# Optimization experiments

Measured on AMD Instinct MI355X. Metric: run time of the kernel, lower is better.

## Reference

```python
import jax, jax.numpy as jnp
import numpy as np

N = 20000      # n_nodes
L = 4          # lamb_len (number of decay rates)
M = 64         # memory_dimension (= message_dimension)
F = 128        # node feature dim
E = 128        # embedding_dimension
B = 100000     # number of interaction events in the batch
RAW = 2 * M * L + F + 1  # 641, raw message dim
H = RAW // 2   # MLP hidden dim


def setup_inputs() -> dict:
    key = jax.random.key(0)
    ks = jax.random.split(key, 18)
    s = lambda d: 1.0 / np.sqrt(d)
    inp = {
        "node_features": jax.random.normal(ks[0], (N, F), jnp.float32),
        "memory": jax.random.normal(ks[1], (N, L, M), jnp.float32) * 0.1,
        "last_update": jnp.zeros((N,), jnp.float32),
        "lambs": jnp.array([1.0, 0.1, 0.01, 0.001], jnp.float32),
        "theta": jnp.array([0.5], jnp.float32),
        "static_emb": jax.random.normal(ks[2], (N, E), jnp.float32),
        "W1": jax.random.normal(ks[3], (H, RAW), jnp.float32) * s(RAW),
        "b1": jnp.zeros((H,), jnp.float32),
        "W2": jax.random.normal(ks[4], (M, H), jnp.float32) * s(H),
        "b2": jnp.zeros((M,), jnp.float32),
        "We": jax.random.normal(ks[5], (M, L * M), jnp.float32) * s(L * M),
        "be": jnp.zeros((M,), jnp.float32),
        "Ws": jax.random.normal(ks[6], (E, M), jnp.float32) * s(M),
        "bs": jnp.zeros((E,), jnp.float32),
        "timestamps": jax.random.uniform(ks[7], (B,), jnp.float32) * 1000.0,
        "source_nodes": jax.random.randint(ks[8], (B,), 0, N),
        "target_nodes": jax.random.randint(ks[9], (B,), 0, N),
    }
    return inp


def reference(node_features, memory, last_update, lambs, theta, static_emb,
              W1, b1, W2, b2, We, be, Ws, bs,
              timestamps, source_nodes, target_nodes):
    n, l, m = memory.shape
    b = source_nodes.shape[0]
    mem_flat = memory.reshape(n, l * m)

    # ---- temporal memory gather + raw message build: [B, RAW] ----
    src_emb = mem_flat[source_nodes]
    tgt_emb = mem_flat[target_nodes]
    raw = jnp.concatenate(
        [src_emb, tgt_emb, node_features[target_nodes],
         jnp.ones((b, 1), memory.dtype)], axis=1)

    # ---- exp_lambs aggregation per source node ----
    t_node = jax.ops.segment_max(timestamps, source_nodes, num_segments=n)
    counts = jax.ops.segment_sum(jnp.ones_like(timestamps), source_nodes,
                                 num_segments=n)
    has = counts > 0
    t_node_safe = jnp.where(has, t_node, last_update)  # latest event time per node
    dt = t_node_safe[source_nodes] - timestamps        # [B], >= 0
    w = jnp.exp(-dt[:, None] * lambs[None, :])         # [B, L] decay weights
    # decayed sum of raw messages per node, per lambda: [N, L, RAW]
    agg = jnp.stack(
        [jax.ops.segment_sum(w[:, li:li + 1] * raw, source_nodes,
                             num_segments=n) for li in range(l)], axis=1)

    # ---- MLP message function: [N, L, M] ----
    h = jax.nn.relu(jnp.einsum('nlr,hr->nlh', agg, W1) + b1)
    msg = jnp.einsum('nlh,mh->nlm', h, W2) + b2

    # ---- exp memory update ----
    decay = jnp.exp(-(t_node_safe - last_update)[:, None] * lambs[None, :])  # [N, L]
    updated = memory * decay[..., None] + jnp.where(has[:, None, None], msg, 0.0)

    # ---- embedding fusion ----
    dyn = updated.reshape(n, l * m)
    e = jax.nn.leaky_relu(dyn @ We.T + be, negative_slope=0.01)
    s = jax.nn.leaky_relu(e @ Ws.T + bs, negative_slope=0.01)
    embeddings = theta * static_emb + (1.0 - theta) * s
    return embeddings
```

## Files before the change

### kernel.cpp

```cpp
#include <hip/hip_runtime.h>

constexpr int LDIM = 4;
constexpr int MDIM = 64;
constexpr int FDIM = 128;
constexpr int EDIM = 128;
constexpr int RAWD = 641;
constexpr int HDIM = 320;
constexpr int LM   = LDIM * MDIM;
constexpr int KXY  = LM + FDIM;
constexpr int NXY  = 2 * HDIM;

typedef _Float16 f16x8 __attribute__((ext_vector_type(8)));
typedef _Float16 f16x4 __attribute__((ext_vector_type(4)));
typedef float    f32x4 __attribute__((ext_vector_type(4)));

constexpr float WSCALE  = 256.f;
constexpr float WSINV   = 1.f / 256.f;

__global__ void k_init(int* t_node_bits, int* counts, int* cursor2, int* cursor, int Nn)
{
    int n = blockIdx.x * blockDim.x + threadIdx.x;
    if (n < Nn) {
        t_node_bits[n] = 0xBF800000;
        counts[n]  = 0;
        cursor2[n] = 0;
    }
    if (n == 0) cursor[0] = 0;
}

__global__ void k_ev1(const int* __restrict__ src, const float* __restrict__ ts,
                      int* t_node_bits, int* counts, int Bev)
{
    int b = blockIdx.x * blockDim.x + threadIdx.x;
    if (b >= Bev) return;
    int s = src[b];
    atomicMax(&t_node_bits[s], __float_as_int(ts[b]));
    atomicAdd(&counts[s], 1);
}

__global__ void k_node(const int* __restrict__ t_node_bits, const int* __restrict__ counts,
                       const float* __restrict__ last_update, const float* __restrict__ lambs,
                       float* t_safe, float* decay, int* start, int* cursor, int Nn)
{
    int n = blockIdx.x * blockDim.x + threadIdx.x;
    if (n >= Nn) return;
    int c = counts[n];
    float lu = last_update[n];
    float tsn = (c > 0) ? __int_as_float(t_node_bits[n]) : lu;
    t_safe[n] = tsn;
    float d = tsn - lu;
    #pragma unroll
    for (int li = 0; li < LDIM; ++li)
        decay[n * LDIM + li] = expf(-d * lambs[li]);
    start[n] = atomicAdd(cursor, c);
}

__global__ void k_ev2(const int* __restrict__ src, const int* __restrict__ tgt,
                      const float* __restrict__ ts, const float* __restrict__ t_safe,
                      const int* __restrict__ start, int* cursor2,
                      const float* __restrict__ lambs,
                      int* sorted_tgt, float4* sorted_w, int Bev)
{
    int b = blockIdx.x * blockDim.x + threadIdx.x;
    if (b >= Bev) return;
    int s = src[b];
    int pos = start[s] + atomicAdd(&cursor2[s], 1);
    sorted_tgt[pos] = tgt[b];
    float dt = t_safe[s] - ts[b];
    sorted_w[pos] = make_float4(expf(-dt * lambs[0]), expf(-dt * lambs[1]),
                                expf(-dt * lambs[2]), expf(-dt * lambs[3]));
}

__global__ void k_prep(const float* __restrict__ W1, const float* __restrict__ W2,
                       const float* __restrict__ We, const float* __restrict__ Ws,
                       const float* __restrict__ mem, const float* __restrict__ nf,
                       _Float16* WpH, _Float16* WpL, _Float16* W2H, _Float16* W2L,
                       _Float16* WeH, _Float16* WeL, _Float16* WsH, _Float16* WsL,
                       _Float16* A1, int packtot)
{
    int idx = blockIdx.x * blockDim.x + threadIdx.x;
    constexpr int T1 = NXY * KXY;
    constexpr int T2 = MDIM * HDIM;
    constexpr int T3 = MDIM * LM;
    constexpr int T4 = EDIM * MDIM;
    constexpr int TW = T1 + T2 + T3 + T4;
    if (idx < TW) {
        float v; _Float16 *H, *L; int o;
        if (idx < T1) {
            int n = idx / KXY, k = idx % KXY;
            if (n < HDIM) {
                v = (k < LM) ? W1[(long)n * RAWD + k] : 0.f;
            } else {
                int hh = n - HDIM;
                v = (k < LM) ? W1[(long)hh * RAWD + LM + k]
                             : W1[(long)hh * RAWD + 2 * LM + (k - LM)];
            }
            H = WpH; L = WpL; o = idx;
        } else if (idx < T1 + T2) {
            o = idx - T1; v = W2[o]; H = W2H; L = W2L;
        } else if (idx < T1 + T2 + T3) {
            o = idx - T1 - T2; v = We[o]; H = WeH; L = WeL;
        } else {
            o = idx - T1 - T2 - T3; v = Ws[o]; H = WsH; L = WsL;
        }
        float xs = WSCALE * v;
        _Float16 hh = (_Float16)xs;
        _Float16 ll = (_Float16)(xs - (float)hh);
        H[o] = hh; L[o] = ll;
    } else {
        int r = idx - TW;
        if (r < packtot) {
            int n = r / KXY, k = r % KXY;
            float v = (k < LM) ? mem[(long)n * LM + k] : nf[(long)n * FDIM + (k - LM)];
            A1[r] = (_Float16)v;
        }
    }
}

__global__ __launch_bounds__(256) void k_gather(
    const _Float16* __restrict__ C1, const float4* __restrict__ sorted_w,
    const int* __restrict__ sorted_tgt, const int* __restrict__ startb,
    const int* __restrict__ counts,
    const float* __restrict__ W1, const float* __restrict__ b1,
    _Float16* __restrict__ h, int Nn)
{
    const int lane = threadIdx.x & 63;
    const int wv   = threadIdx.x >> 6;
    float4 b4 = *(const float4*)&b1[lane * 4];
    float bbA[4] = {b4.x, b4.y, b4.z, b4.w};
    float bbB = b1[256 + lane];
    float wlA[4], wlB;
    #pragma unroll
    for (int j = 0; j < 4; ++j)
        wlA[j] = W1[(long)(lane * 4 + j) * RAWD + (RAWD - 1)];
    wlB = W1[(long)(256 + lane) * RAWD + (RAWD - 1)];

    for (int n = blockIdx.x * 4 + wv; n < Nn; n += gridDim.x * 4) {
        int cnt = counts[n];
        if (cnt == 0) continue;
        int st = startb[n];
        float zA[4][4], zB[4], sw[4];
        #pragma unroll
        for (int li = 0; li < 4; ++li) { zB[li] = 0.f; sw[li] = 0.f; }
        #pragma unroll
        for (int j = 0; j < 4; ++j)
            #pragma unroll
            for (int li = 0; li < 4; ++li) zA[j][li] = 0.f;

        for (int e = 0; e < cnt; ++e) {
            float4 w = sorted_w[st + e];
            int    t = sorted_tgt[st + e];
            const _Float16* yr = C1 + (long)t * NXY + HDIM;
            f16x4 yA = *(const f16x4*)(yr + lane * 4);
            float  yB = (float)yr[256 + lane];
            float wf[4] = {w.x, w.y, w.z, w.w};
            sw[0] += w.x; sw[1] += w.y; sw[2] += w.z; sw[3] += w.w;
            #pragma unroll
            for (int j = 0; j < 4; ++j) {
                float yv = (float)yA[j];
                #pragma unroll
                for (int li = 0; li < 4; ++li) zA[j][li] += wf[li] * yv;
            }
            #pragma unroll
            for (int li = 0; li < 4; ++li) zB[li] += wf[li] * yB;
        }

        const _Float16* xr = C1 + (long)n * NXY;
        f16x4 xA4 = *(const f16x4*)(xr + lane * 4);
        float xB = (float)xr[256 + lane] + wlB;
        float xA[4];
        #pragma unroll
        for (int j = 0; j < 4; ++j) xA[j] = (float)xA4[j] + wlA[j];
        #pragma unroll
        for (int li = 0; li < 4; ++li) {
            _Float16* hr = h + ((long)n * LDIM + li) * HDIM;
            f16x4 hv;
            #pragma unroll
            for (int j = 0; j < 4; ++j)
                hv[j] = (_Float16)fmaxf(xA[j] * sw[li] + zA[j][li] + bbA[j], 0.f);
            *(f16x4*)(hr + lane * 4) = hv;
            hr[256 + lane] = (_Float16)fmaxf(xB * sw[li] + zB[li] + bbB, 0.f);
        }
    }
}

template <int BM, int BN, int WM, int WN, int EPI>
__global__ __launch_bounds__(256) void k_mgemm(
    const _Float16* __restrict__ Ag,
    const _Float16* __restrict__ Bgh, const _Float16* __restrict__ Bgl,
    _Float16* __restrict__ Ch, float* __restrict__ Cf,
    int M, int N, int K,
    const float* __restrict__ bias, const _Float16* __restrict__ x1h,
    const float* __restrict__ x1f, const float* __restrict__ x2,
    const int* __restrict__ icnts, const float* __restrict__ theta)
{
    constexpr int BK = 32;
    constexpr int WROWS = BM / WM, WCOLS = BN / WN;
    constexpr int SM = WROWS / 16, SN = WCOLS / 16;
    static_assert(WM * WN == 4 && SM * 16 == WROWS && SN * 16 == WCOLS, "");
    static_assert((BM * 4) % 256 == 0 && (BN * 4) % 256 == 0, "");
    __shared__ _Float16 Ash[BM * BK];
    __shared__ _Float16 Bsh[BN * BK], Bsl[BN * BK];
    const int tid  = threadIdx.x;
    const int w    = tid >> 6, lane = tid & 63;
    const int wm   = w / WN,   wn   = w % WN;
    const int lrow = lane & 15, lq = lane >> 4;
    const long m0 = (long)blockIdx.x * BM;
    const int  n0 = blockIdx.y * BN;

    f32x4 acc[SM][SN];
    #pragma unroll
    for (int s = 0; s < SM; ++s)
        #pragma unroll
        for (int t = 0; t < SN; ++t) acc[s][t] = (f32x4){0.f, 0.f, 0.f, 0.f};

    for (int k0 = 0; k0 < K; k0 += BK) {
        #pragma unroll
        for (int f0 = 0; f0 < BM * 4; f0 += 256) {
            int c = f0 + tid;
            int row = c >> 2, kc = c & 3;
            long gm = m0 + row; if (gm > M - 1) gm = M - 1;
            int soff = row * BK + ((kc ^ ((row >> 1) & 3)) << 3);
            *(int4*)&Ash[soff] = *(const int4*)(Ag + gm * (long)K + k0 + kc * 8);
        }
        #pragma unroll
        for (int f0 = 0; f0 < BN * 4; f0 += 256) {
            int c = f0 + tid;
            int row = c >> 2, kc = c & 3;
            long goff = (long)(n0 + row) * K + k0 + kc * 8;
            int soff = row * BK + ((kc ^ ((row >> 1) & 3)) << 3);
            *(int4*)&Bsh[soff] = *(const int4*)(Bgh + goff);
            *(int4*)&Bsl[soff] = *(const int4*)(Bgl + goff);
        }
        __syncthreads();

        f16x8 a[SM], bh[SN], bl[SN];
        #pragma unroll
        for (int s = 0; s < SM; ++s) {
            int row = wm * WROWS + s * 16 + lrow;
            a[s] = *(const f16x8*)&Ash[row * BK + ((lq ^ ((row >> 1) & 3)) << 3)];
        }
        #pragma unroll
        for (int t = 0; t < SN; ++t) {
            int row = wn * WCOLS + t * 16 + lrow;
            int off = row * BK + ((lq ^ ((row >> 1) & 3)) << 3);
            bh[t] = *(const f16x8*)&Bsh[off];
            bl[t] = *(const f16x8*)&Bsl[off];
        }
        #pragma unroll
        for (int s = 0; s < SM; ++s)
            #pragma unroll
            for (int t = 0; t < SN; ++t) {
                acc[s][t] = __builtin_amdgcn_mfma_f32_16x16x32_f16(a[s], bh[t], acc[s][t], 0, 0, 0);
                acc[s][t] = __builtin_amdgcn_mfma_f32_16x16x32_f16(a[s], bl[t], acc[s][t], 0, 0, 0);
            }
        __syncthreads();
    }

    float th = 0.f;
    if constexpr (EPI == 3) th = theta[0];
    #pragma unroll
    for (int s = 0; s < SM; ++s) {
        #pragma unroll
        for (int t = 0; t < SN; ++t) {
            #pragma unroll
            for (int r = 0; r < 4; ++r) {
                long grow = m0 + wm * WROWS + s * 16 + lq * 4 + r;
                if (grow >= M) continue;
                int col = n0 + wn * WCOLS + t * 16 + lrow;
                float v = acc[s][t][r] * WSINV;
                long idx = grow * (long)N + col;
                if constexpr (EPI == 0) {
                    Ch[idx] = (_Float16)v;
                } else if constexpr (EPI == 1) {
                    float vb = v + bias[col];
                    bool has = icnts[grow >> 2] > 0;
                    float mv = (float)x1h[(grow >> 2) * KXY + (grow & 3) * MDIM + col];
                    float u = mv * x2[grow] + (has ? vb : 0.f);
                    Ch[idx] = (_Float16)u;
                } else if constexpr (EPI == 2) {
                    float u = v + bias[col];
                    u = u > 0.f ? u : 0.01f * u;
                    Ch[idx] = (_Float16)u;
                } else {
                    float u = v + bias[col];
                    u = u > 0.f ? u : 0.01f * u;
                    Cf[idx] = th * x1f[idx] + (1.f - th) * u;
                }
            }
        }
    }
}

extern "C" void kernel_launch(void* const* d_in, const int* in_sizes, int n_in,
                              void* d_out, int out_size, void* d_ws, size_t ws_size,
                              hipStream_t stream)
{
    (void)n_in; (void)out_size; (void)ws_size;
    const float* node_features = (const float*)d_in[0];
    const float* memory        = (const float*)d_in[1];
    const float* last_update   = (const float*)d_in[2];
    const float* lambs         = (const float*)d_in[3];
    const float* theta         = (const float*)d_in[4];
    const float* static_emb    = (const float*)d_in[5];
    const float* W1            = (const float*)d_in[6];
    const float* b1            = (const float*)d_in[7];
    const float* W2            = (const float*)d_in[8];
    const float* b2            = (const float*)d_in[9];
    const float* We            = (const float*)d_in[10];
    const float* be            = (const float*)d_in[11];
    const float* Ws            = (const float*)d_in[12];
    const float* bs            = (const float*)d_in[13];
    const float* timestamps    = (const float*)d_in[14];
    const int*   src           = (const int*)d_in[15];
    const int*   tgt           = (const int*)d_in[16];
    float* out = (float*)d_out;

    const int Nn  = in_sizes[2];
    const int Bev = in_sizes[14];

    char* base = (char*)d_ws;
    size_t off = 0;
    auto take = [&](size_t bytes) -> void* {
        off = (off + 255) & ~(size_t)255;
        void* r = base + off;
        off += bytes;
        return r;
    };
    int*    t_node_bits = (int*)   take((size_t)Nn * 4);
    int*    counts      = (int*)   take((size_t)Nn * 4);
    int*    startb      = (int*)   take((size_t)Nn * 4);
    int*    cursor2     = (int*)   take((size_t)Nn * 4);
    int*    cursor      = (int*)   take(256);
    float*  t_safe      = (float*) take((size_t)Nn * 4);
    float*  decay       = (float*) take((size_t)Nn * LDIM * 4);
    int*    sorted_tgt  = (int*)   take((size_t)Bev * 4);
    float4* sorted_w    = (float4*)take((size_t)Bev * 16);
    _Float16* WpH = (_Float16*)take((size_t)NXY * KXY * 2);
    _Float16* WpL = (_Float16*)take((size_t)NXY * KXY * 2);
    _Float16* W2H = (_Float16*)take((size_t)MDIM * HDIM * 2);
    _Float16* W2L = (_Float16*)take((size_t)MDIM * HDIM * 2);
    _Float16* WeH = (_Float16*)take((size_t)MDIM * LM * 2);
    _Float16* WeL = (_Float16*)take((size_t)MDIM * LM * 2);
    _Float16* WsH = (_Float16*)take((size_t)EDIM * MDIM * 2);
    _Float16* WsL = (_Float16*)take((size_t)EDIM * MDIM * 2);
    _Float16* A1  = (_Float16*)take((size_t)Nn * KXY * 2);
    _Float16* C1  = (_Float16*)take((size_t)Nn * NXY * 2);
    _Float16* hbuf= (_Float16*)take((size_t)Nn * LDIM * HDIM * 2);
    _Float16* updh= (_Float16*)take((size_t)Nn * LM * 2);
    _Float16* ebuf= (_Float16*)take((size_t)Nn * MDIM * 2);

    const int tb = 256;
    k_init<<<(Nn + tb - 1) / tb, tb, 0, stream>>>(t_node_bits, counts, cursor2, cursor, Nn);
    k_ev1<<<(Bev + tb - 1) / tb, tb, 0, stream>>>(src, timestamps, t_node_bits, counts, Bev);
    k_node<<<(Nn + tb - 1) / tb, tb, 0, stream>>>(t_node_bits, counts, last_update, lambs,
                                                  t_safe, decay, startb, cursor, Nn);
    k_ev2<<<(Bev + tb - 1) / tb, tb, 0, stream>>>(src, tgt, timestamps, t_safe,
                                                  startb, cursor2, lambs,
                                                  sorted_tgt, sorted_w, Bev);
    const int packtot = Nn * KXY;
    const int preptot = NXY * KXY + MDIM * HDIM + MDIM * LM + EDIM * MDIM + packtot;
    k_prep<<<(preptot + tb - 1) / tb, tb, 0, stream>>>(W1, W2, We, Ws,
                                                       memory, node_features,
                                                       WpH, WpL, W2H, W2L,
                                                       WeH, WeL, WsH, WsL,
                                                       A1, packtot);

    const int mb64 = (Nn + 63) / 64;

    k_mgemm<64, 128, 1, 4, 0><<<dim3(mb64, NXY / 128), 256, 0, stream>>>(
        A1, WpH, WpL, C1, nullptr, Nn, NXY, KXY,
        nullptr, nullptr, nullptr, nullptr, nullptr, nullptr);

    k_gather<<<5000, 256, 0, stream>>>(C1, sorted_w, sorted_tgt, startb, counts,
                                       W1, b1, hbuf, Nn);

    k_mgemm<64, 64, 2, 2, 1><<<dim3(Nn * LDIM / 64, 1), 256, 0, stream>>>(
        hbuf, W2H, W2L, updh, nullptr, Nn * LDIM, MDIM, HDIM,
        b2, A1, nullptr, decay, counts, nullptr);

    k_mgemm<64, 64, 2, 2, 2><<<dim3(mb64, 1), 256, 0, stream>>>(
        updh, WeH, WeL, ebuf, nullptr, Nn, MDIM, LM,
        be, nullptr, nullptr, nullptr, nullptr, nullptr);

    k_mgemm<64, 128, 1, 4, 3><<<dim3(mb64, 1), 256, 0, stream>>>(
        ebuf, WsH, WsL, nullptr, out, Nn, EDIM, MDIM,
        bs, nullptr, static_emb, nullptr, nullptr, theta);
}
```

Before: 276.2 us.

## Fuse embedding GEMMs into one tail kernel, vectorize packing, prefetch gather loads

The last two GEMMs (We projection with leaky ReLU, then Ws projection with theta blend) are merged into one kernel that keeps the intermediate 64-wide embedding tile in shared memory. This removes the ebuf round trip through global memory and one launch. The A1 packing in k_prep now converts four floats per thread with vector loads and stores. The gather loop software-prefetches the next event's weight, target and C1 row. The fused tail reads Ws fragments straight from global memory instead of staging them in LDS, and the prefetch uses extra registers.

```diff
diff --git a/kernel.cpp b/kernel.cpp
--- a/kernel.cpp
+++ b/kernel.cpp
@@ -76,7 +76,7 @@
                        const float* __restrict__ mem, const float* __restrict__ nf,
                        _Float16* WpH, _Float16* WpL, _Float16* W2H, _Float16* W2L,
                        _Float16* WeH, _Float16* WeL, _Float16* WsH, _Float16* WsL,
-                       _Float16* A1, int packtot)
+                       _Float16* A1, int packq)
 {
     int idx = blockIdx.x * blockDim.x + threadIdx.x;
     constexpr int T1 = NXY * KXY;
@@ -109,10 +109,13 @@
         H[o] = hh; L[o] = ll;
     } else {
         int r = idx - TW;
-        if (r < packtot) {
-            int n = r / KXY, k = r % KXY;
-            float v = (k < LM) ? mem[(long)n * LM + k] : nf[(long)n * FDIM + (k - LM)];
-            A1[r] = (_Float16)v;
+        if (r < packq) {
+            constexpr int KQ = KXY / 4;
+            int n = r / KQ, kq = r % KQ, k = kq * 4;
+            float4 v = (k < LM) ? *(const float4*)(mem + (long)n * LM + k)
+                                : *(const float4*)(nf  + (long)n * FDIM + (k - LM));
+            f16x4 o4 = {(_Float16)v.x, (_Float16)v.y, (_Float16)v.z, (_Float16)v.w};
+            *(f16x4*)(A1 + (long)n * KXY + k) = o4;
         }
     }
 }
@@ -147,12 +150,21 @@
             #pragma unroll
             for (int li = 0; li < 4; ++li) zA[j][li] = 0.f;
 
+        float4 w0 = sorted_w[st];
+        int    t0 = sorted_tgt[st];
+        const _Float16* yr0 = C1 + (long)t0 * NXY + HDIM;
+        f16x4 yA0 = *(const f16x4*)(yr0 + lane * 4);
+        float  yB0 = (float)yr0[256 + lane];
+
         for (int e = 0; e < cnt; ++e) {
-            float4 w = sorted_w[st + e];
-            int    t = sorted_tgt[st + e];
-            const _Float16* yr = C1 + (long)t * NXY + HDIM;
-            f16x4 yA = *(const f16x4*)(yr + lane * 4);
-            float  yB = (float)yr[256 + lane];
+            float4 w = w0; f16x4 yA = yA0; float yB = yB0;
+            if (e + 1 < cnt) {
+                w0 = sorted_w[st + e + 1];
+                int t1 = sorted_tgt[st + e + 1];
+                const _Float16* yr1 = C1 + (long)t1 * NXY + HDIM;
+                yA0 = *(const f16x4*)(yr1 + lane * 4);
+                yB0 = (float)yr1[256 + lane];
+            }
             float wf[4] = {w.x, w.y, w.z, w.w};
             sw[0] += w.x; sw[1] += w.y; sw[2] += w.z; sw[3] += w.w;
             #pragma unroll
@@ -188,11 +200,10 @@
 __global__ __launch_bounds__(256) void k_mgemm(
     const _Float16* __restrict__ Ag,
     const _Float16* __restrict__ Bgh, const _Float16* __restrict__ Bgl,
-    _Float16* __restrict__ Ch, float* __restrict__ Cf,
+    _Float16* __restrict__ Ch,
     int M, int N, int K,
     const float* __restrict__ bias, const _Float16* __restrict__ x1h,
-    const float* __restrict__ x1f, const float* __restrict__ x2,
-    const int* __restrict__ icnts, const float* __restrict__ theta)
+    const float* __restrict__ x2, const int* __restrict__ icnts)
 {
     constexpr int BK = 32;
     constexpr int WROWS = BM / WM, WCOLS = BN / WN;
@@ -257,8 +268,6 @@
         __syncthreads();
     }
 
-    float th = 0.f;
-    if constexpr (EPI == 3) th = theta[0];
     #pragma unroll
     for (int s = 0; s < SM; ++s) {
         #pragma unroll
@@ -272,23 +281,140 @@
                 long idx = grow * (long)N + col;
                 if constexpr (EPI == 0) {
                     Ch[idx] = (_Float16)v;
-                } else if constexpr (EPI == 1) {
+                } else {
                     float vb = v + bias[col];
                     bool has = icnts[grow >> 2] > 0;
                     float mv = (float)x1h[(grow >> 2) * KXY + (grow & 3) * MDIM + col];
                     float u = mv * x2[grow] + (has ? vb : 0.f);
                     Ch[idx] = (_Float16)u;
-                } else if constexpr (EPI == 2) {
-                    float u = v + bias[col];
+                }
+            }
+        }
+    }
+}
+
+__global__ __launch_bounds__(256) void k_tail(
+    const _Float16* __restrict__ upd,
+    const _Float16* __restrict__ WeH, const _Float16* __restrict__ WeL,
+    const _Float16* __restrict__ WsH, const _Float16* __restrict__ WsL,
+    const float* __restrict__ be, const float* __restrict__ bs,
+    const float* __restrict__ static_emb, const float* __restrict__ theta,
+    float* __restrict__ out, int M)
+{
+    constexpr int BK = 32, EP = 72;
+    __shared__ _Float16 Ash[64 * BK];
+    __shared__ _Float16 Bsh[64 * BK], Bsl[64 * BK];
+    __shared__ _Float16 es[64][EP];
+    const int tid  = threadIdx.x;
+    const int w    = tid >> 6, lane = tid & 63;
+    const int lrow = lane & 15, lq = lane >> 4;
+    const long m0 = (long)blockIdx.x * 64;
+
+    {
+        const int wm = w >> 1, wn = w & 1;
+        f32x4 acc[2][2];
+        #pragma unroll
+        for (int s = 0; s < 2; ++s)
+            #pragma unroll
+            for (int t = 0; t < 2; ++t) acc[s][t] = (f32x4){0.f, 0.f, 0.f, 0.f};
+
+        for (int k0 = 0; k0 < LM; k0 += BK) {
+            {
+                int c = tid;
+                int row = c >> 2, kc = c & 3;
+                long gm = m0 + row; if (gm > M - 1) gm = M - 1;
+                int soff = row * BK + ((kc ^ ((row >> 1) & 3)) << 3);
+                *(int4*)&Ash[soff] = *(const int4*)(upd + gm * (long)LM + k0 + kc * 8);
+                long goff = (long)row * LM + k0 + kc * 8;
+                *(int4*)&Bsh[soff] = *(const int4*)(WeH + goff);
+                *(int4*)&Bsl[soff] = *(const int4*)(WeL + goff);
+            }
+            __syncthreads();
+            f16x8 a[2], bh[2], bl[2];
+            #pragma unroll
+            for (int s = 0; s < 2; ++s) {
+                int row = wm * 32 + s * 16 + lrow;
+                a[s] = *(const f16x8*)&Ash[row * BK + ((lq ^ ((row >> 1) & 3)) << 3)];
+            }
+            #pragma unroll
+            for (int t = 0; t < 2; ++t) {
+                int row = wn * 32 + t * 16 + lrow;
+                int off = row * BK + ((lq ^ ((row >> 1) & 3)) << 3);
+                bh[t] = *(const f16x8*)&Bsh[off];
+                bl[t] = *(const f16x8*)&Bsl[off];
+            }
+            #pragma unroll
+            for (int s = 0; s < 2; ++s)
+                #pragma unroll
+                for (int t = 0; t < 2; ++t) {
+                    acc[s][t] = __builtin_amdgcn_mfma_f32_16x16x32_f16(a[s], bh[t], acc[s][t], 0, 0, 0);
+                    acc[s][t] = __builtin_amdgcn_mfma_f32_16x16x32_f16(a[s], bl[t], acc[s][t], 0, 0, 0);
+                }
+            __syncthreads();
+        }
+        #pragma unroll
+        for (int s = 0; s < 2; ++s)
+            #pragma unroll
+            for (int t = 0; t < 2; ++t) {
+                int col = wn * 32 + t * 16 + lrow;
+                float bb = be[col];
+                #pragma unroll
+                for (int r = 0; r < 4; ++r) {
+                    int row = wm * 32 + s * 16 + lq * 4 + r;
+                    float u = acc[s][t][r] * WSINV + bb;
                     u = u > 0.f ? u : 0.01f * u;
-                    Ch[idx] = (_Float16)u;
-                } else {
-                    float u = v + bias[col];
+                    es[row][col] = (_Float16)u;
+                }
+            }
+    }
+    __syncthreads();
+
+    {
+        f32x4 acc[4][2];
+        #pragma unroll
+        for (int s = 0; s < 4; ++s)
+            #pragma unroll
+            for (int t = 0; t < 2; ++t) acc[s][t] = (f32x4){0.f, 0.f, 0.f, 0.f};
+
+        #pragma unroll
+        for (int k0 = 0; k0 < MDIM; k0 += BK) {
+            f16x8 a[4], bh[2], bl[2];
+            #pragma unroll
+            for (int s = 0; s < 4; ++s)
+                a[s] = *(const f16x8*)&es[s * 16 + lrow][k0 + lq * 8];
+            #pragma unroll
+            for (int t = 0; t < 2; ++t) {
+                int col = w * 32 + t * 16 + lrow;
+                long bo = (long)col * MDIM + k0 + lq * 8;
+                bh[t] = *(const f16x8*)&WsH[bo];
+                bl[t] = *(const f16x8*)&WsL[bo];
+            }
+            #pragma unroll
+            for (int s = 0; s < 4; ++s)
+                #pragma unroll
+                for (int t = 0; t < 2; ++t) {
+                    acc[s][t] = __builtin_amdgcn_mfma_f32_16x16x32_f16(a[s], bh[t], acc[s][t], 0, 0, 0);
+                    acc[s][t] = __builtin_amdgcn_mfma_f32_16x16x32_f16(a[s], bl[t], acc[s][t], 0, 0, 0);
+                }
+        }
+
+        float th = theta[0];
+        #pragma unroll
+        for (int s = 0; s < 4; ++s)
+            #pragma unroll
+            for (int t = 0; t < 2; ++t) {
+                int col = w * 32 + t * 16 + lrow;
+                float bb = bs[col];
+                #pragma unroll
+                for (int r = 0; r < 4; ++r) {
+                    long grow = m0 + s * 16 + lq * 4 + r;
+                    if (grow >= M) continue;
+                    float u = acc[s][t][r] * WSINV + bb;
                     u = u > 0.f ? u : 0.01f * u;
-                    Cf[idx] = th * x1f[idx] + (1.f - th) * u;
+                    long idx = grow * (long)EDIM + col;
+                    out[idx] = th * static_emb[idx] + (1.f - th) * u;
                 }
             }
-        }
     }
 }
 
@@ -348,7 +474,6 @@
     _Float16* C1  = (_Float16*)take((size_t)Nn * NXY * 2);
     _Float16* hbuf= (_Float16*)take((size_t)Nn * LDIM * HDIM * 2);
     _Float16* updh= (_Float16*)take((size_t)Nn * LM * 2);
-    _Float16* ebuf= (_Float16*)take((size_t)Nn * MDIM * 2);
 
     const int tb = 256;
     k_init<<<(Nn + tb - 1) / tb, tb, 0, stream>>>(t_node_bits, counts, cursor2, cursor, Nn);
@@ -358,32 +483,27 @@
     k_ev2<<<(Bev + tb - 1) / tb, tb, 0, stream>>>(src, tgt, timestamps, t_safe,
                                                   startb, cursor2, lambs,
                                                   sorted_tgt, sorted_w, Bev);
-    const int packtot = Nn * KXY;
-    const int preptot = NXY * KXY + MDIM * HDIM + MDIM * LM + EDIM * MDIM + packtot;
+    const int packq = Nn * KXY / 4;
+    const int preptot = NXY * KXY + MDIM * HDIM + MDIM * LM + EDIM * MDIM + packq;
     k_prep<<<(preptot + tb - 1) / tb, tb, 0, stream>>>(W1, W2, We, Ws,
                                                        memory, node_features,
                                                        WpH, WpL, W2H, W2L,
                                                        WeH, WeL, WsH, WsL,
-                                                       A1, packtot);
+                                                       A1, packq);
 
     const int mb64 = (Nn + 63) / 64;
 
     k_mgemm<64, 128, 1, 4, 0><<<dim3(mb64, NXY / 128), 256, 0, stream>>>(
-        A1, WpH, WpL, C1, nullptr, Nn, NXY, KXY,
-        nullptr, nullptr, nullptr, nullptr, nullptr, nullptr);
+        A1, WpH, WpL, C1, Nn, NXY, KXY,
+        nullptr, nullptr, nullptr, nullptr);
 
     k_gather<<<5000, 256, 0, stream>>>(C1, sorted_w, sorted_tgt, startb, counts,
                                        W1, b1, hbuf, Nn);
 
     k_mgemm<64, 64, 2, 2, 1><<<dim3(Nn * LDIM / 64, 1), 256, 0, stream>>>(
-        hbuf, W2H, W2L, updh, nullptr, Nn * LDIM, MDIM, HDIM,
-        b2, A1, nullptr, decay, counts, nullptr);
-
-    k_mgemm<64, 64, 2, 2, 2><<<dim3(mb64, 1), 256, 0, stream>>>(
-        updh, WeH, WeL, ebuf, nullptr, Nn, MDIM, LM,
-        be, nullptr, nullptr, nullptr, nullptr, nullptr);
-
-    k_mgemm<64, 128, 1, 4, 3><<<dim3(mb64, 1), 256, 0, stream>>>(
-        ebuf, WsH, WsL, nullptr, out, Nn, EDIM, MDIM,
-        bs, nullptr, static_emb, nullptr, nullptr, theta);
-}
+        hbuf, W2H, W2L, updh, Nn * LDIM, MDIM, HDIM,
+        b2, A1, decay, counts);
+
+    k_tail<<<mb64, 256, 0, stream>>>(updh, WeH, WeL, WsH, WsL,
+                                     be, bs, static_emb, theta, out, Nn);
+}
```

Result: faster. 262.8 us (-4.9%).
